# Kernel tuning notes

Measured on AMD Instinct MI355X. Metric: run time of the kernel, lower is better.

The kernel has to match this reference:

```python
import jax, jax.numpy as jnp
import numpy as np

B, N, E = 8, 10000, 320000
HIST, PRED = 24, 12
IN_DIM, GNN_OUT, HID = 17, 13, 64


def setup_inputs() -> dict:
    key = jax.random.key(0)
    ks = jax.random.split(key, 16)
    rn = lambda k, s, sc=0.1: jax.random.normal(k, s, jnp.float32) * sc
    return {
        "t2m_hist": jax.random.normal(ks[0], (B, HIST, N, 1), jnp.float32),
        "feature": jax.random.normal(ks[1], (B, HIST + PRED, N, IN_DIM - 1), jnp.float32),
        "edge_index": jax.random.randint(ks[2], (2, E), 0, N),
        "edge_attr": jax.random.normal(ks[3], (E, 1), jnp.float32),
        "edge_w1": rn(ks[4], (2 * IN_DIM + 1, 32)),
        "edge_b1": rn(ks[5], (32,)),
        "edge_w2": rn(ks[6], (32, 30)),
        "edge_b2": rn(ks[7], (30,)),
        "node_w": rn(ks[8], (30, GNN_OUT)),
        "node_b": rn(ks[9], (GNN_OUT,)),
        "gru_wih": rn(ks[10], (3 * HID, IN_DIM + GNN_OUT)),
        "gru_whh": rn(ks[11], (3 * HID, HID)),
        "gru_bih": rn(ks[12], (3 * HID,)),
        "gru_bhh": rn(ks[13], (3 * HID,)),
        "fc_out_w": rn(ks[14], (HID, 1)),
        "fc_out_b": rn(ks[15], (1,)),
    }


def reference(t2m_hist, feature, edge_index, edge_attr,
              edge_w1, edge_b1, edge_w2, edge_b2, node_w, node_b,
              gru_wih, gru_whh, gru_bih, gru_bhh, fc_out_w, fc_out_b):
    src, tgt = edge_index[0], edge_index[1]
    # edge_attr normalized with unbiased std (torch default)
    ea_norm = (edge_attr - edge_attr.mean(0)) / edge_attr.std(0, ddof=1)  # [E,1]

    def graph_gnn(x):  # x: [B,N,IN_DIM]
        ns = x[:, src]                                  # [B,E,IN_DIM] gather
        nt = x[:, tgt]                                  # [B,E,IN_DIM] gather
        ea = jnp.broadcast_to(ea_norm[None], (B, E, 1))
        h = jnp.concatenate([ns, nt, ea], axis=-1)      # [B,E,2*IN_DIM+1]
        h = jax.nn.sigmoid(h @ edge_w1 + edge_b1)
        h = jax.nn.sigmoid(h @ edge_w2 + edge_b2)       # [B,E,30]
        agg = jnp.zeros((B, N, 30), h.dtype)
        agg = agg.at[:, tgt].add(h)                     # scatter_add to targets
        agg = agg.at[:, src].add(-h)                    # scatter_add(-) to sources
        return jax.nn.sigmoid(agg @ node_w + node_b)    # [B,N,GNN_OUT]

    def gru(xin, h):  # xin: [M,30], h: [M,HID]  (PyTorch GRUCell math)
        gi = xin @ gru_wih.T + gru_bih
        gh = h @ gru_whh.T + gru_bhh
        i_r, i_z, i_n = jnp.split(gi, 3, axis=-1)
        h_r, h_z, h_n = jnp.split(gh, 3, axis=-1)
        r = jax.nn.sigmoid(i_r + h_r)
        z = jax.nn.sigmoid(i_z + h_z)
        n = jnp.tanh(i_n + r * h_n)
        return (1.0 - z) * n + z * h

    feat_future = jnp.moveaxis(feature[:, HIST:HIST + PRED], 1, 0)  # [PRED,B,N,16]
    h0 = jnp.zeros((B * N, HID), jnp.float32)
    xn0 = t2m_hist[:, -1]  # [B,N,1]

    def step(carry, feat_t):
        hn, xn = carry
        x = jnp.concatenate([xn, feat_t], axis=-1)      # [B,N,IN_DIM]
        g = graph_gnn(x)                                # [B,N,GNN_OUT]
        xin = jnp.concatenate([g, x], axis=-1).reshape(B * N, IN_DIM + GNN_OUT)
        hn = gru(xin, hn)
        xn = hn.reshape(B, N, HID) @ fc_out_w + fc_out_b  # [B,N,1]
        return (hn, xn), xn

    _, preds = jax.lax.scan(step, (h0, xn0), feat_future)  # [PRED,B,N,1]
    return jnp.moveaxis(preds, 0, 1)                        # [B,PRED,N,1]
```

## Files before the change

### kernel.cpp

```cpp
#include <hip/hip_runtime.h>
#include <hip/hip_fp16.h>
#include <hip/hip_bf16.h>

#define Bb 8
#define Nn 10000
#define Ee 320000
#define HIST 24
#define PRED 12
#define BN (Bb * Nn)

__device__ __forceinline__ float sigm(float x) { return 1.0f / (1.0f + __expf(-x)); }
__device__ __forceinline__ float tanh_fast(float x) { return 1.0f - 2.0f / (__expf(2.0f * x) + 1.0f); }

__device__ __forceinline__ void load16f(const float* p, float* o) {
  const float4* q = reinterpret_cast<const float4*>(p);
  float4 a = q[0], b = q[1], c = q[2], d = q[3];
  o[0] = a.x; o[1] = a.y; o[2]  = a.z; o[3]  = a.w;
  o[4] = b.x; o[5] = b.y; o[6]  = b.z; o[7]  = b.w;
  o[8] = c.x; o[9] = c.y; o[10] = c.z; o[11] = c.w;
  o[12] = d.x; o[13] = d.y; o[14] = d.z; o[15] = d.w;
}

__device__ __forceinline__ void edge_mlp(const float* __restrict__ in,
                                         const float* __restrict__ W,
                                         float* __restrict__ h2) {
  const float* w1 = W;
  const float* b1 = W + 1120;
  const float* w2 = W + 1152;
  const float* b2 = W + 2112;
  float h1[32];
#pragma unroll
  for (int j = 0; j < 32; j++) h1[j] = b1[j];
#pragma unroll
  for (int k = 0; k < 35; k++) {
    float v = in[k];
#pragma unroll
    for (int j = 0; j < 32; j++) h1[j] = fmaf(v, w1[k * 32 + j], h1[j]);
  }
#pragma unroll
  for (int j = 0; j < 32; j++) h1[j] = sigm(h1[j]);
#pragma unroll
  for (int j = 0; j < 30; j++) h2[j] = b2[j];
#pragma unroll
  for (int k = 0; k < 32; k++) {
    float v = h1[k];
#pragma unroll
    for (int j = 0; j < 30; j++) h2[j] = fmaf(v, w2[k * 30 + j], h2[j]);
  }
#pragma unroll
  for (int j = 0; j < 30; j++) h2[j] = sigm(h2[j]);
}

__device__ __forceinline__ void gru_out(const float* __restrict__ agg,
                                        const float* __restrict__ W,
                                        const float* __restrict__ featp,
                                        float xn_old,
                                        float* __restrict__ xn_new_slot,
                                        float* __restrict__ hp,
                                        float* __restrict__ out_slot) {
  const float* nw  = W + 2142;
  const float* nb  = W + 2532;
  const float* wih = W + 2545;
  const float* whh = W + 8305;
  const float* bih = W + 20593;
  const float* bhh = W + 20785;
  const float* fw  = W + 20977;
  const float* fcb = W + 21041;
  float xin[30];
#pragma unroll
  for (int j = 0; j < 13; j++) {
    float a = nb[j];
#pragma unroll
    for (int k = 0; k < 30; k++) a = fmaf(agg[k], nw[k * 13 + j], a);
    xin[j] = sigm(a);
  }
  xin[13] = xn_old;
  load16f(featp, xin + 14);
  float h[64];
#pragma unroll
  for (int j = 0; j < 64; j++) h[j] = hp[j];
  float xnew = fcb[0];
  for (int j = 0; j < 64; j++) {
    float ir = bih[j], iz = bih[64 + j], inn = bih[128 + j];
    const float* wr = wih + j * 30;
    const float* wz = wih + (64 + j) * 30;
    const float* wn = wih + (128 + j) * 30;
#pragma unroll
    for (int k = 0; k < 30; k++) {
      ir  = fmaf(xin[k], wr[k], ir);
      iz  = fmaf(xin[k], wz[k], iz);
      inn = fmaf(xin[k], wn[k], inn);
    }
    float hr = bhh[j], hz = bhh[64 + j], hn_ = bhh[128 + j];
    const float* vr = whh + j * 64;
    const float* vz = whh + (64 + j) * 64;
    const float* vn = whh + (128 + j) * 64;
#pragma unroll
    for (int k = 0; k < 64; k++) {
      hr  = fmaf(h[k], vr[k], hr);
      hz  = fmaf(h[k], vz[k], hz);
      hn_ = fmaf(h[k], vn[k], hn_);
    }
    float rg = sigm(ir + hr);
    float zg = sigm(iz + hz);
    float ng = tanh_fast(inn + rg * hn_);
    float hnew = (1.f - zg) * ng + zg * h[j];
    hp[j] = hnew;
    xnew = fmaf(hnew, fw[j], xnew);
  }
  *xn_new_slot = xnew;
  *out_slot = xnew;
}


__global__ void k_stats(const float* __restrict__ ea, float* __restrict__ stats) {
  __shared__ float s1[256], s2[256];
  int tid = threadIdx.x;
  int i = blockIdx.x * 256 + tid;
  float v = 0.f;
  if (i < Ee) v = ea[i];
  s1[tid] = v;
  s2[tid] = v * v;
  __syncthreads();
  for (int o = 128; o > 0; o >>= 1) {
    if (tid < o) { s1[tid] += s1[tid + o]; s2[tid] += s2[tid + o]; }
    __syncthreads();
  }
  if (tid == 0) { atomicAdd(&stats[0], s1[0]); atomicAdd(&stats[1], s2[0]); }
}

__global__ void k_finalize_stats(float* stats) {
  float sum = stats[0], sumsq = stats[1];
  float mean = sum / (float)Ee;
  float var = (sumsq - sum * mean) / (float)(Ee - 1);
  stats[2] = mean;
  stats[3] = rsqrtf(var);
}

__global__ void k_hist(const int* __restrict__ eidx, int* __restrict__ deg_t, int* __restrict__ deg_s) {
  int e = blockIdx.x * 256 + threadIdx.x;
  if (e >= Ee) return;
  atomicAdd(&deg_s[eidx[e]], 1);
  atomicAdd(&deg_t[eidx[Ee + e]], 1);
}

__global__ void k_scan(const int* __restrict__ deg_t, int* __restrict__ off_t,
                       const int* __restrict__ deg_s, int* __restrict__ off_s) {
  const int* deg = (blockIdx.x == 0) ? deg_t : deg_s;
  int* off = (blockIdx.x == 0) ? off_t : off_s;
  __shared__ int s[1024];
  __shared__ int carry;
  int tid = threadIdx.x;
  if (tid == 0) carry = 0;
  __syncthreads();
  for (int base = 0; base < Nn; base += 1024) {
    int v = (base + tid < Nn) ? deg[base + tid] : 0;
    s[tid] = v;
    int val = v;
    __syncthreads();
    for (int o = 1; o < 1024; o <<= 1) {
      int tv = (tid >= o) ? s[tid - o] : 0;
      __syncthreads();
      val += tv;
      s[tid] = val;
      __syncthreads();
    }
    if (base + tid < Nn) off[base + tid] = carry + (val - v);
    __syncthreads();
    if (tid == 1023) carry += val;
    __syncthreads();
  }
  if (tid == 0) off[Nn] = carry;
}

__global__ void k_fill(const int* __restrict__ eidx,
                       const int* __restrict__ off_t, const int* __restrict__ off_s,
                       int* __restrict__ cur_t, int* __restrict__ cur_s,
                       int* __restrict__ list_t, int* __restrict__ list_s) {
  int e = blockIdx.x * 256 + threadIdx.x;
  if (e >= Ee) return;
  int s = eidx[e], t = eidx[Ee + e];
  int ps = off_s[s] + atomicAdd(&cur_s[s], 1);
  list_s[ps] = e;
  int pt = off_t[t] + atomicAdd(&cur_t[t], 1);
  list_t[pt] = e;
}

__global__ void k_convert(const float* w1, const float* b1, const float* w2, const float* b2,
                          const float* nw, const float* nb, const float* wih, const float* whh,
                          const float* bih, const float* bhh, const float* fw, const float* fb,
                          float* __restrict__ dst) {
  int i = blockIdx.x * 256 + threadIdx.x;
  const int c1 = 1120, c2 = 1152, c3 = 2112, c4 = 2142, c5 = 2532, c6 = 2545,
            c7 = 8305, c8 = 20593, c9 = 20785, c10 = 20977, c11 = 21041, c12 = 21042;
  if (i >= c12) return;
  const float* p;
  int base;
  if (i < c1)       { p = w1;  base = 0;  }
  else if (i < c2)  { p = b1;  base = c1; }
  else if (i < c3)  { p = w2;  base = c2; }
  else if (i < c4)  { p = b2;  base = c3; }
  else if (i < c5)  { p = nw;  base = c4; }
  else if (i < c6)  { p = nb;  base = c5; }
  else if (i < c7)  { p = wih; base = c6; }
  else if (i < c8)  { p = whh; base = c7; }
  else if (i < c9)  { p = bih; base = c8; }
  else if (i < c10) { p = bhh; base = c9; }
  else if (i < c11) { p = fw;  base = c10; }
  else              { p = fb;  base = c11; }
  dst[i] = p[i - base];
}

__global__ void k_xn0(const float* __restrict__ t2m, float* __restrict__ xn) {
  int i = blockIdx.x * 256 + threadIdx.x;
  if (i >= BN) return;
  int b = i / Nn, n = i % Nn;
  xn[i] = t2m[((size_t)b * HIST + (HIST - 1)) * Nn + n];
}


__global__ __launch_bounds__(256) void k_pre_edge(
    const float* __restrict__ feat, const float* __restrict__ xn,
    const float* __restrict__ W, float* __restrict__ as_, float* __restrict__ at_, int t) {
  int idx = blockIdx.x * 256 + threadIdx.x;
  if (idx >= BN) return;
  int b = idx / Nn, n = idx % Nn;
  const float* w1 = W;
  const float* b1 = W + 1120;
  float f[16];
  const float* fbp = feat + ((size_t)(b * (HIST + PRED) + HIST + t)) * Nn * 16 + (size_t)n * 16;
  load16f(fbp, f);
  float x = xn[idx];
  float as[32], at[32];
#pragma unroll
  for (int j = 0; j < 32; j++) {
    as[j] = fmaf(x, w1[j], b1[j]);
    at[j] = x * w1[17 * 32 + j];
  }
#pragma unroll
  for (int k = 0; k < 16; k++) {
    float v = f[k];
#pragma unroll
    for (int j = 0; j < 32; j++) {
      as[j] = fmaf(v, w1[(1 + k) * 32 + j], as[j]);
      at[j] = fmaf(v, w1[(18 + k) * 32 + j], at[j]);
    }
  }
  float4* ap = (float4*)(as_ + (size_t)idx * 32);
  float4* bp = (float4*)(at_ + (size_t)idx * 32);
#pragma unroll
  for (int q = 0; q < 8; q++) {
    ap[q] = make_float4(as[4 * q], as[4 * q + 1], as[4 * q + 2], as[4 * q + 3]);
    bp[q] = make_float4(at[4 * q], at[4 * q + 1], at[4 * q + 2], at[4 * q + 3]);
  }
}

__global__ __launch_bounds__(256) void k_edge2(
    const int* __restrict__ eidx, const float* __restrict__ ea,
    const float* __restrict__ as_, const float* __restrict__ at_,
    const float* __restrict__ W, const float* __restrict__ stats,
    __half* __restrict__ h2p) {
  int e = blockIdx.x * 256 + threadIdx.x;
  int b = blockIdx.y;
  if (e >= Ee) return;
  float mean = stats[2], istd = stats[3];
  int s = eidx[e], tg = eidx[Ee + e];
  float ean = (ea[e] - mean) * istd;
  const float* w1e = W + 34 * 32;
  const float* w2 = W + 1152;
  const float* b2 = W + 2112;
  const float4* ap = (const float4*)(as_ + ((size_t)(b * Nn + s)) * 32);
  const float4* bp = (const float4*)(at_ + ((size_t)(b * Nn + tg)) * 32);
  float h1[32];
#pragma unroll
  for (int q = 0; q < 8; q++) {
    float4 av = ap[q], bv = bp[q];
    h1[4 * q]     = av.x + bv.x;
    h1[4 * q + 1] = av.y + bv.y;
    h1[4 * q + 2] = av.z + bv.z;
    h1[4 * q + 3] = av.w + bv.w;
  }
#pragma unroll
  for (int j = 0; j < 32; j++) h1[j] = sigm(fmaf(ean, w1e[j], h1[j]));
  float h2[30];
#pragma unroll
  for (int j = 0; j < 30; j++) h2[j] = b2[j];
#pragma unroll
  for (int k = 0; k < 32; k++) {
    float v = h1[k];
#pragma unroll
    for (int j = 0; j < 30; j++) h2[j] = fmaf(v, w2[k * 30 + j], h2[j]);
  }
  __half2* o = (__half2*)(h2p + (size_t)e * 240 + b * 30);
#pragma unroll
  for (int i = 0; i < 15; i++) o[i] = __floats2half2_rn(sigm(h2[2 * i]), sigm(h2[2 * i + 1]));
}

__global__ __launch_bounds__(256) void k_gather8(
    const int* __restrict__ off_t, const int* __restrict__ list_t,
    const int* __restrict__ off_s, const int* __restrict__ list_s,
    const __half* __restrict__ h2p, float* __restrict__ agg) {
  const int lane = threadIdx.x & 63;
  const int wave = threadIdx.x >> 6;
  const int n = blockIdx.x * 4 + wave;
  const bool hasP1 = (lane < 56);

  float a0x = 0.f, a0y = 0.f, a1x = 0.f, a1y = 0.f;

  int p0 = off_t[n], p1 = off_t[n + 1];
  int p = p0;
  for (; p + 2 <= p1; p += 2) {
    int e0 = list_t[p], e1 = list_t[p + 1];
    const __half2* r0 = (const __half2*)(h2p + (size_t)e0 * 240);
    const __half2* r1 = (const __half2*)(h2p + (size_t)e1 * 240);
    __half2 u0 = r0[lane];
    __half2 v0 = r1[lane];
    __half2 u1 = hasP1 ? r0[lane + 64] : __half2{};
    __half2 v1 = hasP1 ? r1[lane + 64] : __half2{};
    a0x += __low2float(u0) + __low2float(v0);
    a0y += __high2float(u0) + __high2float(v0);
    a1x += __low2float(u1) + __low2float(v1);
    a1y += __high2float(u1) + __high2float(v1);
  }
  for (; p < p1; p++) {
    int e0 = list_t[p];
    const __half2* r0 = (const __half2*)(h2p + (size_t)e0 * 240);
    __half2 u0 = r0[lane];
    __half2 u1 = hasP1 ? r0[lane + 64] : __half2{};
    a0x += __low2float(u0); a0y += __high2float(u0);
    a1x += __low2float(u1); a1y += __high2float(u1);
  }
  p0 = off_s[n]; p1 = off_s[n + 1];
  p = p0;
  for (; p + 2 <= p1; p += 2) {
    int e0 = list_s[p], e1 = list_s[p + 1];
    const __half2* r0 = (const __half2*)(h2p + (size_t)e0 * 240);
    const __half2* r1 = (const __half2*)(h2p + (size_t)e1 * 240);
    __half2 u0 = r0[lane];
    __half2 v0 = r1[lane];
    __half2 u1 = hasP1 ? r0[lane + 64] : __half2{};
    __half2 v1 = hasP1 ? r1[lane + 64] : __half2{};
    a0x -= __low2float(u0) + __low2float(v0);
    a0y -= __high2float(u0) + __high2float(v0);
    a1x -= __low2float(u1) + __low2float(v1);
    a1y -= __high2float(u1) + __high2float(v1);
  }
  for (; p < p1; p++) {
    int e0 = list_s[p];
    const __half2* r0 = (const __half2*)(h2p + (size_t)e0 * 240);
    __half2 u0 = r0[lane];
    __half2 u1 = hasP1 ? r0[lane + 64] : __half2{};
    a0x -= __low2float(u0); a0y -= __high2float(u0);
    a1x -= __low2float(u1); a1y -= __high2float(u1);
  }

  {
    int b0 = lane / 15, c0 = (lane % 15) * 2;
    *(float2*)(agg + ((size_t)b0 * Nn + n) * 30 + c0) = make_float2(a0x, a0y);
    if (hasP1) {
      int P1i = lane + 64;
      int b1 = P1i / 15, c1 = (P1i % 15) * 2;
      *(float2*)(agg + ((size_t)b1 * Nn + n) * 30 + c1) = make_float2(a1x, a1y);
    }
  }
}

__global__ __launch_bounds__(256) void k_edge(
    const int* __restrict__ eidx, const float* __restrict__ ea,
    const float* __restrict__ feat, const float* __restrict__ xn,
    const float* __restrict__ W, const float* __restrict__ stats,
    __half* __restrict__ h2out, int t) {
  int e = blockIdx.x * 256 + threadIdx.x;
  int b = blockIdx.y;
  if (e >= Ee) return;
  float mean = stats[2], istd = stats[3];
  int s = eidx[e], tg = eidx[Ee + e];
  float in[35];
  in[0]  = xn[b * Nn + s];
  in[17] = xn[b * Nn + tg];
  in[34] = (ea[e] - mean) * istd;
  const float* fb = feat + ((size_t)(b * (HIST + PRED) + HIST + t)) * Nn * 16;
  load16f(fb + (size_t)s * 16, in + 1);
  load16f(fb + (size_t)tg * 16, in + 18);
  float h2[30];
  edge_mlp(in, W, h2);
  __half2* o = (__half2*)(h2out + ((size_t)b * Ee + e) * 30);
#pragma unroll
  for (int i = 0; i < 15; i++) o[i] = __floats2half2_rn(h2[2 * i], h2[2 * i + 1]);
}

__global__ __launch_bounds__(256) void k_gather(
    const int* __restrict__ off_t, const int* __restrict__ list_t,
    const int* __restrict__ off_s, const int* __restrict__ list_s,
    const __half* __restrict__ h2, float* __restrict__ agg) {
  int tid = threadIdx.x;
  int c = tid & 31;
  int idx = blockIdx.x * 8 + (tid >> 5);
  if (idx >= BN || c >= 30) return;
  int b = idx / Nn, n = idx % Nn;
  const __half* base = h2 + (size_t)b * Ee * 30;
  float a = 0.f;
  int p0 = off_t[n], p1 = off_t[n + 1];
  int p = p0;
  for (; p + 4 <= p1; p += 4) {
    int e0 = list_t[p], e1 = list_t[p + 1], e2 = list_t[p + 2], e3 = list_t[p + 3];
    float v0 = __half2float(base[(size_t)e0 * 30 + c]);
    float v1 = __half2float(base[(size_t)e1 * 30 + c]);
    float v2 = __half2float(base[(size_t)e2 * 30 + c]);
    float v3 = __half2float(base[(size_t)e3 * 30 + c]);
    a += (v0 + v1) + (v2 + v3);
  }
  for (; p < p1; p++) a += __half2float(base[(size_t)list_t[p] * 30 + c]);
  p0 = off_s[n]; p1 = off_s[n + 1];
  p = p0;
  for (; p + 4 <= p1; p += 4) {
    int e0 = list_s[p], e1 = list_s[p + 1], e2 = list_s[p + 2], e3 = list_s[p + 3];
    float v0 = __half2float(base[(size_t)e0 * 30 + c]);
    float v1 = __half2float(base[(size_t)e1 * 30 + c]);
    float v2 = __half2float(base[(size_t)e2 * 30 + c]);
    float v3 = __half2float(base[(size_t)e3 * 30 + c]);
    a -= (v0 + v1) + (v2 + v3);
  }
  for (; p < p1; p++) a -= __half2float(base[(size_t)list_s[p] * 30 + c]);
  agg[(size_t)idx * 30 + c] = a;
}

#define HS_STRIDE 68

__global__ __launch_bounds__(256, 4) void k_gru4(
    const float* __restrict__ agg_all, const float* __restrict__ W,
    const float* __restrict__ feat, const float* __restrict__ xn_cur,
    float* __restrict__ xn_nxt, float* __restrict__ hbuf,
    float* __restrict__ out, int t) {
  __shared__ float hs[64 * HS_STRIDE];
  __shared__ float sx[4][64];

  const int tid = threadIdx.x;
  const int lane = tid & 63;
  const int wave = (int)__builtin_amdgcn_readfirstlane(tid >> 6);
  const int node = blockIdx.x * 64 + lane;
  const int b = node / Nn, n = node % Nn;

  const float* nw  = W + 2142;
  const float* nb  = W + 2532;
  const float* wih = W + 2545;
  const float* whh = W + 8305;
  const float* bih = W + 20593;
  const float* bhh = W + 20785;
  const float* fw  = W + 20977;
  const float* fcb = W + 21041;

  float* hp = hbuf + node;
  {
    const int k0 = wave * 16;
#pragma unroll
    for (int kk = 0; kk < 16; kk++) {
      int k = k0 + kk;
      hs[lane * HS_STRIDE + k] = hp[(size_t)k * BN];
    }
  }

  float xin[30];
  {
    float agg[30];
    const float* ap = agg_all + (size_t)node * 30;
#pragma unroll
    for (int i = 0; i < 30; i++) agg[i] = ap[i];
#pragma unroll
    for (int j = 0; j < 13; j++) {
      float a = nb[j];
#pragma unroll
      for (int k = 0; k < 30; k++) a = fmaf(agg[k], nw[k * 13 + j], a);
      xin[j] = sigm(a);
    }
  }
  xin[13] = xn_cur[node];
  const float* fbp = feat + ((size_t)(b * (HIST + PRED) + HIST + t)) * Nn * 16 + (size_t)n * 16;
  load16f(fbp, xin + 14);

  __syncthreads();

  const int j0 = wave * 16;
  const float* hrow = hs + lane * HS_STRIDE;
  float xpart = 0.f;
  for (int jj = 0; jj < 16; jj++) {
    const int j = j0 + jj;
    float ir = bih[j], iz = bih[64 + j], inn = bih[128 + j];
    const float* wr = wih + j * 30;
    const float* wz = wih + (64 + j) * 30;
    const float* wn = wih + (128 + j) * 30;
#pragma unroll
    for (int k = 0; k < 30; k++) {
      ir  = fmaf(xin[k], wr[k], ir);
      iz  = fmaf(xin[k], wz[k], iz);
      inn = fmaf(xin[k], wn[k], inn);
    }
    float hr = bhh[j], hz = bhh[64 + j], hn_ = bhh[128 + j];
    const float* vr = whh + j * 64;
    const float* vz = whh + (64 + j) * 64;
    const float* vn = whh + (128 + j) * 64;
#pragma unroll
    for (int k4 = 0; k4 < 16; k4++) {
      float4 h4 = *reinterpret_cast<const float4*>(hrow + k4 * 4);
      hr  = fmaf(h4.x, vr[4 * k4],     hr);
      hz  = fmaf(h4.x, vz[4 * k4],     hz);
      hn_ = fmaf(h4.x, vn[4 * k4],     hn_);
      hr  = fmaf(h4.y, vr[4 * k4 + 1], hr);
      hz  = fmaf(h4.y, vz[4 * k4 + 1], hz);
      hn_ = fmaf(h4.y, vn[4 * k4 + 1], hn_);
      hr  = fmaf(h4.z, vr[4 * k4 + 2], hr);
      hz  = fmaf(h4.z, vz[4 * k4 + 2], hz);
      hn_ = fmaf(h4.z, vn[4 * k4 + 2], hn_);
      hr  = fmaf(h4.w, vr[4 * k4 + 3], hr);
      hz  = fmaf(h4.w, vz[4 * k4 + 3], hz);
      hn_ = fmaf(h4.w, vn[4 * k4 + 3], hn_);
    }
    float holdj = hrow[j];
    float rg = sigm(ir + hr);
    float zg = sigm(iz + hz);
    float ng = tanh_fast(inn + rg * hn_);
    float hnew = (1.f - zg) * ng + zg * holdj;
    hp[(size_t)j * BN] = hnew;
    xpart = fmaf(hnew, fw[j], xpart);
  }

  sx[wave][lane] = xpart;
  __syncthreads();
  if (wave == 0) {
    float xnew = fcb[0] + ((sx[0][lane] + sx[1][lane]) + (sx[2][lane] + sx[3][lane]));
    xn_nxt[node] = xnew;
    out[((size_t)b * PRED + t) * Nn + n] = xnew;
  }
}


__global__ __launch_bounds__(64) void k_node_g(
    const int* __restrict__ off_t, const int* __restrict__ list_t,
    const int* __restrict__ off_s, const int* __restrict__ list_s,
    const __half* __restrict__ h2, const float* __restrict__ W,
    const float* __restrict__ feat, const float* __restrict__ xn_cur,
    float* __restrict__ xn_nxt,
    float* __restrict__ hbuf, float* __restrict__ out, int t) {
  int n = blockIdx.x * 64 + threadIdx.x;
  int b = blockIdx.y;
  if (n >= Nn) return;
  float agg[30];
#pragma unroll
  for (int i = 0; i < 30; i++) agg[i] = 0.f;
  int p0 = off_t[n], p1 = off_t[n + 1];
  for (int p = p0; p < p1; p++) {
    int e = list_t[p];
    const __half2* r = (const __half2*)(h2 + ((size_t)b * Ee + e) * 30);
#pragma unroll
    for (int i = 0; i < 15; i++) {
      __half2 v = r[i];
      agg[2 * i]     += __low2float(v);
      agg[2 * i + 1] += __high2float(v);
    }
  }
  p0 = off_s[n]; p1 = off_s[n + 1];
  for (int p = p0; p < p1; p++) {
    int e = list_s[p];
    const __half2* r = (const __half2*)(h2 + ((size_t)b * Ee + e) * 30);
#pragma unroll
    for (int i = 0; i < 15; i++) {
      __half2 v = r[i];
      agg[2 * i]     -= __low2float(v);
      agg[2 * i + 1] -= __high2float(v);
    }
  }
  const float* fbp = feat + ((size_t)(b * (HIST + PRED) + HIST + t)) * Nn * 16 + (size_t)n * 16;
  gru_out(agg, W, fbp, xn_cur[b * Nn + n], &xn_nxt[b * Nn + n],
          hbuf + ((size_t)b * Nn + n) * 64, &out[((size_t)b * PRED + t) * Nn + n]);
}


__global__ __launch_bounds__(128) void k_node_rc(
    const int* __restrict__ eidx, const float* __restrict__ ea,
    const int* __restrict__ off_t, const int* __restrict__ list_t,
    const int* __restrict__ off_s, const int* __restrict__ list_s,
    const float* __restrict__ W, const float* __restrict__ stats,
    const float* __restrict__ feat, const float* __restrict__ xn_cur,
    float* __restrict__ xn_nxt,
    float* __restrict__ hbuf, float* __restrict__ out, int t) {
  int idx = blockIdx.x * 128 + threadIdx.x;
  if (idx >= BN) return;
  int b = idx / Nn, n = idx % Nn;
  float mean = stats[2], istd = stats[3];
  const float* fslice = feat + ((size_t)(b * (HIST + PRED) + HIST + t)) * Nn * 16;
  float xo = xn_cur[b * Nn + n];
  float fo[16];
  load16f(fslice + (size_t)n * 16, fo);
  float agg[30];
#pragma unroll
  for (int i = 0; i < 30; i++) agg[i] = 0.f;
  float in[35], h2e[30];
  int p0 = off_t[n], p1 = off_t[n + 1];
  for (int p = p0; p < p1; p++) {
    int e = list_t[p];
    int s = eidx[e];
    in[0] = xn_cur[b * Nn + s];
    load16f(fslice + (size_t)s * 16, in + 1);
    in[17] = xo;
#pragma unroll
    for (int i = 0; i < 16; i++) in[18 + i] = fo[i];
    in[34] = (ea[e] - mean) * istd;
    edge_mlp(in, W, h2e);
#pragma unroll
    for (int i = 0; i < 30; i++) agg[i] += h2e[i];
  }
  p0 = off_s[n]; p1 = off_s[n + 1];
  for (int p = p0; p < p1; p++) {
    int e = list_s[p];
    int tg = eidx[Ee + e];
    in[0] = xo;
#pragma unroll
    for (int i = 0; i < 16; i++) in[1 + i] = fo[i];
    in[17] = xn_cur[b * Nn + tg];
    load16f(fslice + (size_t)tg * 16, in + 18);
    in[34] = (ea[e] - mean) * istd;
    edge_mlp(in, W, h2e);
#pragma unroll
    for (int i = 0; i < 30; i++) agg[i] -= h2e[i];
  }
  gru_out(agg, W, fslice + (size_t)n * 16, xo, &xn_nxt[b * Nn + n],
          hbuf + ((size_t)b * Nn + n) * 64, &out[((size_t)b * PRED + t) * Nn + n]);
}


extern "C" void kernel_launch(void* const* d_in, const int* in_sizes, int n_in,
                              void* d_out, int out_size, void* d_ws, size_t ws_size,
                              hipStream_t stream) {
  const float* t2m  = (const float*)d_in[0];
  const float* feat = (const float*)d_in[1];
  const int*   eidx = (const int*)d_in[2];
  const float* ea   = (const float*)d_in[3];
  const float* w1   = (const float*)d_in[4];
  const float* b1   = (const float*)d_in[5];
  const float* w2   = (const float*)d_in[6];
  const float* b2   = (const float*)d_in[7];
  const float* nw   = (const float*)d_in[8];
  const float* nb   = (const float*)d_in[9];
  const float* wih  = (const float*)d_in[10];
  const float* whh  = (const float*)d_in[11];
  const float* bih  = (const float*)d_in[12];
  const float* bhh  = (const float*)d_in[13];
  const float* fw   = (const float*)d_in[14];
  const float* fb   = (const float*)d_in[15];
  float* out = (float*)d_out;

  float* ws = (float*)d_ws;
  float* stats = ws;
  int* deg_t = (int*)(ws + 4);
  int* deg_s = deg_t + Nn;
  int* cur_t = deg_s + Nn;
  int* cur_s = cur_t + Nn;
  float* hbuf = (float*)(cur_s + Nn);
  int* off_t = (int*)(hbuf + (size_t)BN * 64);
  int* off_s = off_t + (Nn + 1);
  int* list_t = off_s + (Nn + 1);
  int* list_s = list_t + Ee;
  float* Wf = (float*)(list_s + Ee);
  float* xnA = Wf + 21056;
  float* xnB = xnA + BN;
  float* base_end = xnB + BN;
  size_t base_bytes = (size_t)((char*)base_end - (char*)d_ws);
  base_bytes = (base_bytes + 15) & ~(size_t)15;
  __half* h2buf = (__half*)((char*)d_ws + base_bytes);
  size_t mid_bytes = base_bytes + (size_t)Bb * Ee * 30 * sizeof(__half);
  mid_bytes = (mid_bytes + 15) & ~(size_t)15;
  float* aggbuf = (float*)((char*)d_ws + mid_bytes);
  size_t big_bytes = mid_bytes + (size_t)BN * 30 * sizeof(float);
  big_bytes = (big_bytes + 15) & ~(size_t)15;
  float* asbuf = (float*)((char*)d_ws + big_bytes);
  float* atbuf = asbuf + (size_t)BN * 32;
  size_t need_big2 = big_bytes + 2 * (size_t)BN * 32 * sizeof(float);
  bool big2 = ws_size >= need_big2;
  bool big  = ws_size >= big_bytes;
  bool mid  = ws_size >= mid_bytes;

  size_t zero_bytes = (size_t)(4 + 4 * Nn + (size_t)BN * 64) * 4;
  hipMemsetAsync(d_ws, 0, zero_bytes, stream);

  k_stats<<<dim3((Ee + 255) / 256), 256, 0, stream>>>(ea, stats);
  k_finalize_stats<<<1, 1, 0, stream>>>(stats);
  k_hist<<<dim3((Ee + 255) / 256), 256, 0, stream>>>(eidx, deg_t, deg_s);
  k_scan<<<2, 1024, 0, stream>>>(deg_t, off_t, deg_s, off_s);
  k_fill<<<dim3((Ee + 255) / 256), 256, 0, stream>>>(eidx, off_t, off_s, cur_t, cur_s, list_t, list_s);
  k_convert<<<dim3((21042 + 255) / 256), 256, 0, stream>>>(w1, b1, w2, b2, nw, nb, wih, whh, bih, bhh, fw, fb, Wf);
  k_xn0<<<dim3((BN + 255) / 256), 256, 0, stream>>>(t2m, xnA);

  for (int t = 0; t < PRED; t++) {
    float* xc  = (t & 1) ? xnB : xnA;
    float* xnx = (t & 1) ? xnA : xnB;
    if (big2) {
      k_pre_edge<<<dim3((BN + 255) / 256), 256, 0, stream>>>(feat, xc, Wf, asbuf, atbuf, t);
      k_edge2<<<dim3((Ee + 255) / 256, Bb), 256, 0, stream>>>(eidx, ea, asbuf, atbuf, Wf, stats, h2buf);
      k_gather8<<<dim3(Nn / 4), 256, 0, stream>>>(off_t, list_t, off_s, list_s, h2buf, aggbuf);
      k_gru4<<<dim3(BN / 64), 256, 0, stream>>>(aggbuf, Wf, feat, xc, xnx, hbuf, out, t);
    } else if (big) {
      k_edge<<<dim3((Ee + 255) / 256, Bb), 256, 0, stream>>>(eidx, ea, feat, xc, Wf, stats, h2buf, t);
      k_gather<<<dim3((BN + 7) / 8), 256, 0, stream>>>(off_t, list_t, off_s, list_s, h2buf, aggbuf);
      k_gru4<<<dim3(BN / 64), 256, 0, stream>>>(aggbuf, Wf, feat, xc, xnx, hbuf, out, t);
    } else if (mid) {
      k_edge<<<dim3((Ee + 255) / 256, Bb), 256, 0, stream>>>(eidx, ea, feat, xc, Wf, stats, h2buf, t);
      k_node_g<<<dim3((Nn + 63) / 64, Bb), 64, 0, stream>>>(off_t, list_t, off_s, list_s, h2buf, Wf, feat, xc, xnx, hbuf, out, t);
    } else {
      k_node_rc<<<dim3((BN + 127) / 128), 128, 0, stream>>>(eidx, ea, off_t, list_t, off_s, list_s, Wf, stats, feat, xc, xnx, hbuf, out, t);
    }
  }
}
```

Measured before the change: 5.410 ms.

## Compute edge MLP second layer with fp16 MFMA via shared-memory staging

Replaces the per-thread scalar 32x30 FMA loop in the edge kernel with MFMA 16x16x32 f16 matrix instructions. Each wave stages its 64 edges' first-layer activations in shared memory as fp16, runs the MFMAs, then writes the sigmoid outputs back to LDS so each edge's 30 halves can be stored contiguously. The intent is to move the dominant ALU cost onto matrix cores. In exchange the first-layer activations and W2 are rounded to fp16 before the matmul, and the kernel adds LDS traffic and block barriers.

```diff
diff --git a/kernel.cpp b/kernel.cpp
--- a/kernel.cpp
+++ b/kernel.cpp
@@ -8,6 +8,11 @@
 #define HIST 24
 #define PRED 12
 #define BN (Bb * Nn)
+
+typedef _Float16 f16;
+typedef __attribute__((ext_vector_type(4))) _Float16 f16x4;
+typedef __attribute__((ext_vector_type(8))) _Float16 f16x8;
+typedef __attribute__((ext_vector_type(4))) float f32x4;
 
 __device__ __forceinline__ float sigm(float x) { return 1.0f / (1.0f + __expf(-x)); }
 __device__ __forceinline__ float tanh_fast(float x) { return 1.0f - 2.0f / (__expf(2.0f * x) + 1.0f); }
@@ -255,45 +260,86 @@
   }
 }
 
-__global__ __launch_bounds__(256) void k_edge2(
+#define H1S 36
+
+__global__ __launch_bounds__(256) void k_edge2m(
     const int* __restrict__ eidx, const float* __restrict__ ea,
     const float* __restrict__ as_, const float* __restrict__ at_,
     const float* __restrict__ W, const float* __restrict__ stats,
     __half* __restrict__ h2p) {
-  int e = blockIdx.x * 256 + threadIdx.x;
-  int b = blockIdx.y;
-  if (e >= Ee) return;
-  float mean = stats[2], istd = stats[3];
-  int s = eidx[e], tg = eidx[Ee + e];
-  float ean = (ea[e] - mean) * istd;
-  const float* w1e = W + 34 * 32;
-  const float* w2 = W + 1152;
-  const float* b2 = W + 2112;
-  const float4* ap = (const float4*)(as_ + ((size_t)(b * Nn + s)) * 32);
-  const float4* bp = (const float4*)(at_ + ((size_t)(b * Nn + tg)) * 32);
-  float h1[32];
-#pragma unroll
-  for (int q = 0; q < 8; q++) {
-    float4 av = ap[q], bv = bp[q];
-    h1[4 * q]     = av.x + bv.x;
-    h1[4 * q + 1] = av.y + bv.y;
-    h1[4 * q + 2] = av.z + bv.z;
-    h1[4 * q + 3] = av.w + bv.w;
-  }
-#pragma unroll
-  for (int j = 0; j < 32; j++) h1[j] = sigm(fmaf(ean, w1e[j], h1[j]));
-  float h2[30];
-#pragma unroll
-  for (int j = 0; j < 30; j++) h2[j] = b2[j];
-#pragma unroll
-  for (int k = 0; k < 32; k++) {
-    float v = h1[k];
-#pragma unroll
-    for (int j = 0; j < 30; j++) h2[j] = fmaf(v, w2[k * 30 + j], h2[j]);
-  }
-  __half2* o = (__half2*)(h2p + (size_t)e * 240 + b * 30);
-#pragma unroll
-  for (int i = 0; i < 15; i++) o[i] = __floats2half2_rn(sigm(h2[2 * i]), sigm(h2[2 * i + 1]));
+  __shared__ f16 h1s[4 * 64 * H1S];
+  const int tid = threadIdx.x;
+  const int lane = tid & 63;
+  const int wave = tid >> 6;
+  const int e = blockIdx.x * 256 + wave * 64 + lane;
+  const int b = blockIdx.y;
+  const float mean = stats[2], istd = stats[3];
+  const float* w1e = W + 1088;
+  const float* w2  = W + 1152;
+  const float* b2  = W + 2112;
+
+  f16* hw = h1s + wave * 64 * H1S;
+  const int q  = lane >> 4;
+  const int cc = lane & 15;
+
+  f16x8 bf0, bf1;
+#pragma unroll
+  for (int i = 0; i < 8; i++) {
+    int k = 8 * q + i;
+    bf0[i] = (f16)w2[k * 30 + cc];
+    bf1[i] = (16 + cc < 30) ? (f16)w2[k * 30 + 16 + cc] : (f16)0.f;
+  }
+
+  {
+    int s = eidx[e], tg = eidx[Ee + e];
+    float ean = (ea[e] - mean) * istd;
+    const float4* ap = (const float4*)(as_ + ((size_t)(b * Nn + s)) * 32);
+    const float4* bp = (const float4*)(at_ + ((size_t)(b * Nn + tg)) * 32);
+    f16* dst = hw + lane * H1S;
+#pragma unroll
+    for (int q8 = 0; q8 < 8; q8++) {
+      float4 av = ap[q8], bv = bp[q8];
+      f16x4 h4;
+      h4[0] = (f16)sigm(fmaf(ean, w1e[4 * q8],     av.x + bv.x));
+      h4[1] = (f16)sigm(fmaf(ean, w1e[4 * q8 + 1], av.y + bv.y));
+      h4[2] = (f16)sigm(fmaf(ean, w1e[4 * q8 + 2], av.z + bv.z));
+      h4[3] = (f16)sigm(fmaf(ean, w1e[4 * q8 + 3], av.w + bv.w));
+      *(f16x4*)(dst + 4 * q8) = h4;
+    }
+  }
+  __syncthreads();
+
+  f32x4 z = {0.f, 0.f, 0.f, 0.f};
+  f32x4 acc0[4], acc1[4];
+#pragma unroll
+  for (int rt = 0; rt < 4; rt++) {
+    const f16* ap = hw + (rt * 16 + cc) * H1S + 8 * q;
+    f16x4 alo = *(const f16x4*)(ap);
+    f16x4 ahi = *(const f16x4*)(ap + 4);
+    f16x8 afrag = __builtin_shufflevector(alo, ahi, 0, 1, 2, 3, 4, 5, 6, 7);
+    acc0[rt] = __builtin_amdgcn_mfma_f32_16x16x32_f16(afrag, bf0, z, 0, 0, 0);
+    acc1[rt] = __builtin_amdgcn_mfma_f32_16x16x32_f16(afrag, bf1, z, 0, 0, 0);
+  }
+
+  float b2c0 = b2[cc];
+  float b2c1 = (16 + cc < 30) ? b2[16 + cc] : 0.f;
+  __syncthreads();
+#pragma unroll
+  for (int rt = 0; rt < 4; rt++) {
+#pragma unroll
+    for (int r = 0; r < 4; r++) {
+      int item = rt * 16 + q * 4 + r;
+      hw[item * H1S + cc] = (f16)sigm(acc0[rt][r] + b2c0);
+      if (16 + cc < 30) hw[item * H1S + 16 + cc] = (f16)sigm(acc1[rt][r] + b2c1);
+    }
+  }
+  __syncthreads();
+  {
+    const unsigned int* src = (const unsigned int*)(hw + lane * H1S);
+    unsigned int* o = (unsigned int*)(h2p + (size_t)e * 240 + b * 30);
+#pragma unroll
+    for (int i = 0; i < 15; i++) o[i] = src[i];
+  }
 }
 
 __global__ __launch_bounds__(256) void k_gather8(
@@ -695,7 +741,7 @@
     float* xnx = (t & 1) ? xnA : xnB;
     if (big2) {
       k_pre_edge<<<dim3((BN + 255) / 256), 256, 0, stream>>>(feat, xc, Wf, asbuf, atbuf, t);
-      k_edge2<<<dim3((Ee + 255) / 256, Bb), 256, 0, stream>>>(eidx, ea, asbuf, atbuf, Wf, stats, h2buf);
+      k_edge2m<<<dim3(Ee / 256, Bb), 256, 0, stream>>>(eidx, ea, asbuf, atbuf, Wf, stats, h2buf);
       k_gather8<<<dim3(Nn / 4), 256, 0, stream>>>(off_t, list_t, off_s, list_s, h2buf, aggbuf);
       k_gru4<<<dim3(BN / 64), 256, 0, stream>>>(aggbuf, Wf, feat, xc, xnx, hbuf, out, t);
     } else if (big) {
```

Result: no change. 5.482 ms (+1.3%).
